# Kernel tuning notes

Measured on AMD Instinct MI355X. Metric: run time of the kernel, lower is better.

The kernel has to match this reference:

```python
import jax, jax.numpy as jnp
import numpy as np


def log_g(x):
    # log of g(x) = where(x>=0, x+0.5, sigmoid(x)) in log space
    return jnp.where(x >= 0, jnp.log(jax.nn.relu(x) + 0.5), -jax.nn.softplus(-x))


def setup_inputs() -> dict:
    key = jax.random.key(0)
    k1, k2, k3 = jax.random.split(key, 3)
    B, S, D = 4, 4096, 2048
    D_INNER = int(D * 1.5)  # 3072
    x = jax.random.normal(k1, (B, S, D), dtype=jnp.float32)
    w_hg = jax.random.normal(k2, (D, 2 * D_INNER), dtype=jnp.float32) * (D ** -0.5)
    w_out = jax.random.normal(k3, (D_INNER, D), dtype=jnp.float32) * (D_INNER ** -0.5)
    return {"x": x, "w_hg": w_hg, "w_out": w_out}


def reference(x, w_hg, w_out):
    # x: [B,S,D]; w_hg: [D, 2*Di]; w_out: [Di, D]
    hg = jnp.einsum('bsd,de->bse', x, w_hg)
    hidden, gate = jnp.split(hg, 2, axis=-1)  # each [B,S,Di]
    log_coeffs = -jax.nn.softplus(gate)        # log(1 - z)
    log_z = -jax.nn.softplus(-gate)            # log z
    log_values = log_z + log_g(hidden)
    # Heinsen associative scan in log space along seq axis
    a_star = jnp.cumsum(log_coeffs, axis=1)
    log_h = a_star + jax.lax.cumlogsumexp(log_values - a_star, axis=1)
    h = jnp.exp(log_h)                         # [B,S,Di]
    out = jnp.einsum('bse,ed->bsd', h, w_out)  # to_out Linear (expansion != 1)
    return out
```

## Files before the change

### kernel.cpp

```cpp
#include <hip/hip_runtime.h>
#include <hip/hip_bf16.h>
#include <stdint.h>

typedef __hip_bfloat16 bf16;
typedef __attribute__((ext_vector_type(8))) short short8;
typedef __attribute__((ext_vector_type(4))) float floatx4;
typedef __attribute__((address_space(3))) const unsigned short lu16;

__device__ __forceinline__ float ldf(const float* p) { return *p; }
__device__ __forceinline__ float ldf(const bf16* p) { return __bfloat162float(*p); }

__device__ __forceinline__ unsigned short f2bu(float f) {
  bf16 b = __float2bfloat16(f);
  return *reinterpret_cast<unsigned short*>(&b);
}

__device__ __forceinline__ void stnt(float* p, float v) { __builtin_nontemporal_store(v, p); }
__device__ __forceinline__ void stnt(bf16* p, float v) {
  __builtin_nontemporal_store(f2bu(v), (unsigned short*)p);
}

__device__ __forceinline__ void ld4(const float* p, float* o) {
  float4 v = *(const float4*)p;
  o[0] = v.x; o[1] = v.y; o[2] = v.z; o[3] = v.w;
}
__device__ __forceinline__ void ld4(const bf16* p, float* o) {
  ushort4 v = *(const ushort4*)p;
  o[0] = __bfloat162float(*(bf16*)&v.x);
  o[1] = __bfloat162float(*(bf16*)&v.y);
  o[2] = __bfloat162float(*(bf16*)&v.z);
  o[3] = __bfloat162float(*(bf16*)&v.w);
}

__device__ __forceinline__ void gl_lds16(const bf16* g, bf16* l) {
  __builtin_amdgcn_global_load_lds((const __attribute__((address_space(1))) void*)g,
                                   (__attribute__((address_space(3))) void*)l,
                                   16, 0, 0);
}

template <int OFF>
__device__ __forceinline__ short8 ldsro(lu16* p) {
  short8 r;
  asm volatile("ds_read_b128 %0, %1 offset:%2" : "=v"(r) : "v"(p), "i"(OFF));
  return r;
}

#define BAR() __builtin_amdgcn_s_barrier()
#define LGKM0() do { asm volatile("s_waitcnt lgkmcnt(0)" ::: "memory"); \
                     __builtin_amdgcn_sched_barrier(0); } while (0)
#define VMCNT(n) asm volatile("s_waitcnt vmcnt(" #n ")" ::: "memory")

__global__ void cvt_f32_bf16(const float* __restrict__ in, bf16* __restrict__ out, long n4) {
  long i = (long)blockIdx.x * blockDim.x + threadIdx.x;
  if (i >= n4) return;
  float4 v = ((const float4*)in)[i];
  ushort4 o;
  o.x = f2bu(v.x); o.y = f2bu(v.y); o.z = f2bu(v.z); o.w = f2bu(v.w);
  ((ushort4*)out)[i] = o;
}

__global__ void transpose_f32_to_bf16(const float* __restrict__ in, bf16* __restrict__ out,
                                      int R, int Cc) {
  __shared__ float tile[32][33];
  int tx = threadIdx.x & 31;
  int ty = threadIdx.x >> 5;
  int c0 = blockIdx.x * 32;
  int r0 = blockIdx.y * 32;
#pragma unroll
  for (int i = 0; i < 32; i += 8)
    tile[ty + i][tx] = in[(long)(r0 + ty + i) * Cc + c0 + tx];
  __syncthreads();
#pragma unroll
  for (int i = 0; i < 32; i += 8)
    out[(long)(c0 + ty + i) * R + r0 + tx] = __float2bfloat16(tile[tx][ty + i]);
}

template <typename OUT_T>
__global__ __launch_bounds__(512, 2) void gemm256(const bf16* __restrict__ A,
                                                  const bf16* __restrict__ BT,
                                                  OUT_T* __restrict__ C,
                                                  int M, int N, int K) {
  __shared__ __align__(16) bf16 lds[2][2][256][64];

  const int tid = threadIdx.x;
  const int w = tid >> 6;
  const int lane = tid & 63;
  const int quad = lane >> 4;
  const int r16 = lane & 15;
  const int wm = (w >> 2) * 128;
  const int wn = (w & 3) * 64;

  const int nbx = N >> 8;
  const int nwg = nbx * (M >> 8);
  const int bid = blockIdx.x;
  const int swz = (bid & 7) * (nwg >> 3) + (bid >> 3);
  const long bM = (long)(swz / nbx) * 256;
  const long bN = (long)(swz % nbx) * 256;

  const int r0 = tid >> 3;
  const int c8 = (tid & 7) ^ (r0 & 7);
  const bf16* Ag = A + (bM + r0) * (long)K + c8 * 8;
  const bf16* Bg = BT + (bN + r0) * (long)K + c8 * 8;
  const int lslot = w * 512;

  bf16* Am0 = &lds[0][0][0][0];
  bf16* Am1 = &lds[1][0][0][0];
  bf16* Bm0 = &lds[0][1][0][0];
  bf16* Bm1 = &lds[1][1][0][0];

  auto stage = [&](const bf16* g, bf16* lmat, int half, int kt) {
    const bf16* gs = g + (long)half * 128 * K + (long)kt * 64;
    bf16* ls = lmat + half * 8192 + lslot;
    gl_lds16(gs, ls);
    gl_lds16(gs + 64L * K, ls + 4096);
  };

  const int lofsA = (wm + r16) * 64;
  const int lofsB = (wn + r16) * 64;
  const int c8x0 = ((0 * 4 + quad) ^ (r16 & 7)) * 8;
  const int c8x1 = ((1 * 4 + quad) ^ (r16 & 7)) * 8;
  lu16* lb = (lu16*)&lds[0][0][0][0];
  lu16* pA0k0 = lb + 0 * 32768 + 0 * 16384 + lofsA + c8x0;
  lu16* pA0k1 = lb + 0 * 32768 + 0 * 16384 + lofsA + c8x1;
  lu16* pA1k0 = lb + 1 * 32768 + 0 * 16384 + lofsA + c8x0;
  lu16* pA1k1 = lb + 1 * 32768 + 0 * 16384 + lofsA + c8x1;
  lu16* pB0k0 = lb + 0 * 32768 + 1 * 16384 + lofsB + c8x0;
  lu16* pB0k1 = lb + 0 * 32768 + 1 * 16384 + lofsB + c8x1;
  lu16* pB1k0 = lb + 1 * 32768 + 1 * 16384 + lofsB + c8x0;
  lu16* pB1k1 = lb + 1 * 32768 + 1 * 16384 + lofsB + c8x1;

  floatx4 acc[8][4];
#pragma unroll
  for (int a = 0; a < 8; a++)
#pragma unroll
    for (int b = 0; b < 4; b++) acc[a][b] = (floatx4){0.f, 0.f, 0.f, 0.f};

  short8 af[4][2], bq0[2][2], bq1[2][2];

#define READ_A(P0, P1, MG) do { \
  af[0][0] = ldsro<((MG)*4 + 0) * 2048>(P0); af[0][1] = ldsro<((MG)*4 + 0) * 2048>(P1); \
  af[1][0] = ldsro<((MG)*4 + 1) * 2048>(P0); af[1][1] = ldsro<((MG)*4 + 1) * 2048>(P1); \
  af[2][0] = ldsro<((MG)*4 + 2) * 2048>(P0); af[2][1] = ldsro<((MG)*4 + 2) * 2048>(P1); \
  af[3][0] = ldsro<((MG)*4 + 3) * 2048>(P0); af[3][1] = ldsro<((MG)*4 + 3) * 2048>(P1); \
} while (0)

#define READ_B(P0, P1, NG, BQ) do { \
  BQ[0][0] = ldsro<((NG)*2 + 0) * 2048>(P0); BQ[0][1] = ldsro<((NG)*2 + 0) * 2048>(P1); \
  BQ[1][0] = ldsro<((NG)*2 + 1) * 2048>(P0); BQ[1][1] = ldsro<((NG)*2 + 1) * 2048>(P1); \
} while (0)

#define PH_MMA(MG, NG, BQ) do { \
  __builtin_amdgcn_s_setprio(1); \
  _Pragma("unroll") \
  for (int mf = 0; mf < 4; ++mf) \
    _Pragma("unroll") \
    for (int nf = 0; nf < 2; ++nf) { \
      acc[(MG)*4 + mf][(NG)*2 + nf] = __builtin_amdgcn_mfma_f32_16x16x32_bf16( \
          af[mf][0], BQ[nf][0], acc[(MG)*4 + mf][(NG)*2 + nf], 0, 0, 0); \
      acc[(MG)*4 + mf][(NG)*2 + nf] = __builtin_amdgcn_mfma_f32_16x16x32_bf16( \
          af[mf][1], BQ[nf][1], acc[(MG)*4 + mf][(NG)*2 + nf], 0, 0, 0); \
    } \
  __builtin_amdgcn_s_setprio(0); \
} while (0)

#define KTILE(PA0, PA1, PB0, PB1, S1, S2, S3, S4, VMX) do { \
  READ_A(PA0, PA1, 0); READ_B(PB0, PB1, 0, bq0); S1; \
  BAR(); LGKM0(); PH_MMA(0, 0, bq0); BAR(); \
  READ_B(PB0, PB1, 1, bq1); S2; \
  BAR(); LGKM0(); PH_MMA(0, 1, bq1); BAR(); \
  READ_A(PA0, PA1, 1); S3; \
  BAR(); LGKM0(); PH_MMA(1, 1, bq1); BAR(); \
  S4; BAR(); PH_MMA(1, 0, bq0); VMX; BAR(); \
} while (0)

  stage(Ag, Am0, 0, 0); stage(Ag, Am0, 1, 0);
  stage(Bg, Bm0, 0, 0); stage(Bg, Bm0, 1, 0);
  stage(Bg, Bm1, 0, 1); stage(Bg, Bm1, 1, 1);
  VMCNT(4);
  BAR();

  const int NI = K >> 7;
  for (int i = 0; i < NI - 1; ++i) {
    const int k1 = 2 * i + 1, k2 = 2 * i + 2, k3 = 2 * i + 3;
    KTILE(pA0k0, pA0k1, pB0k0, pB0k1,
          stage(Ag, Am1, 0, k1), stage(Ag, Am1, 1, k1),
          stage(Bg, Bm0, 0, k2), stage(Bg, Bm0, 1, k2), VMCNT(4));
    KTILE(pA1k0, pA1k1, pB1k0, pB1k1,
          stage(Ag, Am0, 0, k2), stage(Ag, Am0, 1, k2),
          stage(Bg, Bm1, 0, k3), stage(Bg, Bm1, 1, k3), VMCNT(4));
  }
  {
    const int kl = 2 * NI - 1;
    KTILE(pA0k0, pA0k1, pB0k0, pB0k1,
          stage(Ag, Am1, 0, kl), stage(Ag, Am1, 1, kl),
          (void)0, (void)0, VMCNT(0));
    KTILE(pA1k0, pA1k1, pB1k0, pB1k1,
          (void)0, (void)0, (void)0, (void)0, (void)0);
  }

#undef KTILE
#undef PH_MMA
#undef READ_B
#undef READ_A

#pragma unroll
  for (int mf = 0; mf < 8; ++mf) {
#pragma unroll
    for (int i2 = 0; i2 < 4; ++i2) {
      long row = bM + wm + mf * 16 + quad * 4 + i2;
      OUT_T* crow = C + row * (long)N + bN + wn + r16;
#pragma unroll
      for (int nf = 0; nf < 4; ++nf) stnt(&crow[nf * 16], acc[mf][nf][i2]);
    }
  }
}

__device__ __forceinline__ void cv_compute(float hval, float gval, float& c, float& v) {
  float eg = __expf(gval);
  c = 1.f / (1.f + eg);
  float z = 1.f - c;
  float gx = (hval >= 0.f) ? (hval + 0.5f) : (1.f / (1.f + __expf(-hval)));
  v = z * gx;
}

template <typename T>
__global__ void scan_pass1(const T* __restrict__ hg, float* __restrict__ P,
                           float* __restrict__ V, int S, int Di, int NN, int nch) {
  int tid = blockIdx.x * blockDim.x + threadIdx.x;
  int De = Di >> 2;
  int e = (tid % De) * 4;
  int rest = tid / De;
  int ch = rest % nch;
  int b = rest / nch;
  int CH = S / nch;
  const T* ph = hg + ((long)(b * S + ch * CH)) * NN + e;
  float Pv[4] = {1.f, 1.f, 1.f, 1.f}, Vv[4] = {0.f, 0.f, 0.f, 0.f};
  for (int t = 0; t < CH; t++) {
    float hv[4], gv[4];
    ld4(ph, hv);
    ld4(ph + Di, gv);
#pragma unroll
    for (int j = 0; j < 4; j++) {
      float c, v;
      cv_compute(hv[j], gv[j], c, v);
      Pv[j] *= c;
      Vv[j] = fmaf(c, Vv[j], v);
    }
    ph += NN;
  }
  long base = ((long)(b * nch + ch)) * Di + e;
  *(float4*)&P[base] = make_float4(Pv[0], Pv[1], Pv[2], Pv[3]);
  *(float4*)&V[base] = make_float4(Vv[0], Vv[1], Vv[2], Vv[3]);
}

__global__ void scan_pass2(const float* __restrict__ P, const float* __restrict__ V,
                           float* __restrict__ Hc, int Di, int nch) {
  int tid = blockIdx.x * blockDim.x + threadIdx.x;
  int e = tid % Di;
  int b = tid / Di;
  float H = 0.f;
  for (int j = 0; j < nch; j++) {
    long idx = ((long)(b * nch + j)) * Di + e;
    Hc[idx] = H;
    H = fmaf(P[idx], H, V[idx]);
  }
}

template <typename T>
__global__ void scan_pass3(const T* __restrict__ hg, const float* __restrict__ Hc,
                           bf16* __restrict__ h, int S, int Di, int NN, int nch) {
  int tid = blockIdx.x * blockDim.x + threadIdx.x;
  int De = Di >> 2;
  int e = (tid % De) * 4;
  int rest = tid / De;
  int ch = rest % nch;
  int b = rest / nch;
  int CH = S / nch;
  const T* ph = hg + ((long)(b * S + ch * CH)) * NN + e;
  bf16* po = h + ((long)(b * S + ch * CH)) * Di + e;
  long base = ((long)(b * nch + ch)) * Di + e;
  float4 hc = *(const float4*)&Hc[base];
  float H[4] = {hc.x, hc.y, hc.z, hc.w};
  for (int t = 0; t < CH; t++) {
    float hv[4], gv[4];
    ld4(ph, hv);
    ld4(ph + Di, gv);
    ushort4 o;
#pragma unroll
    for (int j = 0; j < 4; j++) {
      float c, v;
      cv_compute(hv[j], gv[j], c, v);
      H[j] = fmaf(c, H[j], v);
    }
    o.x = f2bu(H[0]); o.y = f2bu(H[1]); o.z = f2bu(H[2]); o.w = f2bu(H[3]);
    *(ushort4*)po = o;
    ph += NN;
    po += Di;
  }
}

extern "C" void kernel_launch(void* const* d_in, const int* in_sizes, int n_in,
                              void* d_out, int out_size, void* d_ws, size_t ws_size,
                              hipStream_t stream) {
  const int B = 4, S = 4096, D = 2048, Di = 3072, NN = 6144;
  const int Mr = B * S;
  const int NCH = 32;

  const float* x = (const float*)d_in[0];
  const float* w_hg = (const float*)d_in[1];
  const float* w_out = (const float*)d_in[2];
  float* out = (float*)d_out;

  char* wp = (char*)d_ws;
  bf16* x_bf = (bf16*)wp;  wp += (size_t)Mr * D * 2;
  bf16* whgT = (bf16*)wp;  wp += (size_t)NN * D * 2;
  bf16* woutT = (bf16*)wp; wp += (size_t)D * Di * 2;
  bf16* h_bf = (bf16*)wp;  wp += (size_t)Mr * Di * 2;
  float* P = (float*)wp;   wp += (size_t)B * NCH * Di * 4;
  float* V = (float*)wp;   wp += (size_t)B * NCH * Di * 4;
  float* Hc = (float*)wp;  wp += (size_t)B * NCH * Di * 4;
  size_t used = (size_t)(wp - (char*)d_ws);
  bool f32hg = (used + (size_t)Mr * NN * 4) <= ws_size;
  void* hgp = (void*)wp;

  cvt_f32_bf16<<<(int)(((long)Mr * D / 4 + 255) / 256), 256, 0, stream>>>(x, x_bf, (long)Mr * D / 4);
  transpose_f32_to_bf16<<<dim3(NN / 32, D / 32), 256, 0, stream>>>(w_hg, whgT, D, NN);
  transpose_f32_to_bf16<<<dim3(D / 32, Di / 32), 256, 0, stream>>>(w_out, woutT, Di, D);

  const int nwg1 = (NN / 256) * (Mr / 256);
  const int nwg2 = (D / 256) * (Mr / 256);
  int scan_vthreads = B * NCH * (Di / 4);

  if (f32hg) {
    float* hg = (float*)hgp;
    gemm256<float><<<nwg1, 512, 0, stream>>>(x_bf, whgT, hg, Mr, NN, D);
    scan_pass1<float><<<scan_vthreads / 256, 256, 0, stream>>>(hg, P, V, S, Di, NN, NCH);
    scan_pass2<<<(B * Di) / 256, 256, 0, stream>>>(P, V, Hc, Di, NCH);
    scan_pass3<float><<<scan_vthreads / 256, 256, 0, stream>>>(hg, Hc, h_bf, S, Di, NN, NCH);
  } else {
    bf16* hg = (bf16*)hgp;
    gemm256<bf16><<<nwg1, 512, 0, stream>>>(x_bf, whgT, hg, Mr, NN, D);
    scan_pass1<bf16><<<scan_vthreads / 256, 256, 0, stream>>>(hg, P, V, S, Di, NN, NCH);
    scan_pass2<<<(B * Di) / 256, 256, 0, stream>>>(P, V, Hc, Di, NCH);
    scan_pass3<bf16><<<scan_vthreads / 256, 256, 0, stream>>>(hg, Hc, h_bf, S, Di, NN, NCH);
  }

  gemm256<float><<<nwg2, 512, 0, stream>>>(h_bf, woutT, out, Mr, D, Di);
}
```

Measured before the change: 1.023 ms.

## Always store hg as bf16, rebalance GEMM staging, double scan chunks

Removes the fp32 hg path so the first GEMM always writes bf16 and the scan passes read half the bytes. It also reschedules the GEMM's global-to-LDS staging so one A sub-tile load is issued a phase earlier, with the wait count raised from 4 to 6. Epilogue stores change from nontemporal to regular stores, scan chunks go from 32 to 64, and the P/V/Hc buffers now reuse the x_bf workspace. The cost is lower precision in hg and a shift in the GEMM's prefetch depth and LDS timing.

Measured after the change: 951.7 us. 7.0% less time.

```diff
diff --git a/kernel.cpp b/kernel.cpp
--- a/kernel.cpp
+++ b/kernel.cpp
@@ -7,23 +7,14 @@
 typedef __attribute__((ext_vector_type(4))) float floatx4;
 typedef __attribute__((address_space(3))) const unsigned short lu16;
 
-__device__ __forceinline__ float ldf(const float* p) { return *p; }
-__device__ __forceinline__ float ldf(const bf16* p) { return __bfloat162float(*p); }
-
 __device__ __forceinline__ unsigned short f2bu(float f) {
   bf16 b = __float2bfloat16(f);
   return *reinterpret_cast<unsigned short*>(&b);
 }
 
-__device__ __forceinline__ void stnt(float* p, float v) { __builtin_nontemporal_store(v, p); }
-__device__ __forceinline__ void stnt(bf16* p, float v) {
-  __builtin_nontemporal_store(f2bu(v), (unsigned short*)p);
-}
-
-__device__ __forceinline__ void ld4(const float* p, float* o) {
-  float4 v = *(const float4*)p;
-  o[0] = v.x; o[1] = v.y; o[2] = v.z; o[3] = v.w;
-}
+__device__ __forceinline__ void stf(float* p, float v) { *p = v; }
+__device__ __forceinline__ void stf(bf16* p, float v) { *p = __float2bfloat16(v); }
+
 __device__ __forceinline__ void ld4(const bf16* p, float* o) {
   ushort4 v = *(const ushort4*)p;
   o[0] = __bfloat162float(*(bf16*)&v.x);
@@ -163,37 +154,40 @@
   __builtin_amdgcn_s_setprio(0); \
 } while (0)
 
-#define KTILE(PA0, PA1, PB0, PB1, S1, S2, S3, S4, VMX) do { \
+#define KTILE(PA0, PA1, PB0, PB1, S1, S3, S4a, S4b, VMX) do { \
   READ_A(PA0, PA1, 0); READ_B(PB0, PB1, 0, bq0); S1; \
   BAR(); LGKM0(); PH_MMA(0, 0, bq0); BAR(); \
-  READ_B(PB0, PB1, 1, bq1); S2; \
+  READ_B(PB0, PB1, 1, bq1); \
   BAR(); LGKM0(); PH_MMA(0, 1, bq1); BAR(); \
   READ_A(PA0, PA1, 1); S3; \
   BAR(); LGKM0(); PH_MMA(1, 1, bq1); BAR(); \
-  S4; BAR(); PH_MMA(1, 0, bq0); VMX; BAR(); \
+  S4a; S4b; BAR(); PH_MMA(1, 0, bq0); VMX; BAR(); \
 } while (0)
 
   stage(Ag, Am0, 0, 0); stage(Ag, Am0, 1, 0);
   stage(Bg, Bm0, 0, 0); stage(Bg, Bm0, 1, 0);
-  stage(Bg, Bm1, 0, 1); stage(Bg, Bm1, 1, 1);
-  VMCNT(4);
+  stage(Bg, Bm1, 0, 1);
+  stage(Bg, Bm1, 1, 1); stage(Ag, Am1, 0, 1);
+  VMCNT(6);
   BAR();
 
   const int NI = K >> 7;
   for (int i = 0; i < NI - 1; ++i) {
     const int k1 = 2 * i + 1, k2 = 2 * i + 2, k3 = 2 * i + 3;
     KTILE(pA0k0, pA0k1, pB0k0, pB0k1,
-          stage(Ag, Am1, 0, k1), stage(Ag, Am1, 1, k1),
-          stage(Bg, Bm0, 0, k2), stage(Bg, Bm0, 1, k2), VMCNT(4));
+          stage(Ag, Am1, 1, k1),
+          stage(Bg, Bm0, 0, k2),
+          stage(Bg, Bm0, 1, k2), stage(Ag, Am0, 0, k2), VMCNT(6));
     KTILE(pA1k0, pA1k1, pB1k0, pB1k1,
-          stage(Ag, Am0, 0, k2), stage(Ag, Am0, 1, k2),
-          stage(Bg, Bm1, 0, k3), stage(Bg, Bm1, 1, k3), VMCNT(4));
+          stage(Ag, Am0, 1, k2),
+          stage(Bg, Bm1, 0, k3),
+          stage(Bg, Bm1, 1, k3), stage(Ag, Am1, 0, k3), VMCNT(6));
   }
   {
     const int kl = 2 * NI - 1;
     KTILE(pA0k0, pA0k1, pB0k0, pB0k1,
-          stage(Ag, Am1, 0, kl), stage(Ag, Am1, 1, kl),
-          (void)0, (void)0, VMCNT(0));
+          stage(Ag, Am1, 1, kl),
+          (void)0, (void)0, (void)0, VMCNT(0));
     KTILE(pA1k0, pA1k1, pB1k0, pB1k1,
           (void)0, (void)0, (void)0, (void)0, (void)0);
   }
@@ -210,7 +204,7 @@
       long row = bM + wm + mf * 16 + quad * 4 + i2;
       OUT_T* crow = C + row * (long)N + bN + wn + r16;
 #pragma unroll
-      for (int nf = 0; nf < 4; ++nf) stnt(&crow[nf * 16], acc[mf][nf][i2]);
+      for (int nf = 0; nf < 4; ++nf) stf(&crow[nf * 16], acc[mf][nf][i2]);
     }
   }
 }
@@ -223,8 +217,7 @@
   v = z * gx;
 }
 
-template <typename T>
-__global__ void scan_pass1(const T* __restrict__ hg, float* __restrict__ P,
+__global__ void scan_pass1(const bf16* __restrict__ hg, float* __restrict__ P,
                            float* __restrict__ V, int S, int Di, int NN, int nch) {
   int tid = blockIdx.x * blockDim.x + threadIdx.x;
   int De = Di >> 2;
@@ -233,7 +226,7 @@
   int ch = rest % nch;
   int b = rest / nch;
   int CH = S / nch;
-  const T* ph = hg + ((long)(b * S + ch * CH)) * NN + e;
+  const bf16* ph = hg + ((long)(b * S + ch * CH)) * NN + e;
   float Pv[4] = {1.f, 1.f, 1.f, 1.f}, Vv[4] = {0.f, 0.f, 0.f, 0.f};
   for (int t = 0; t < CH; t++) {
     float hv[4], gv[4];
@@ -266,8 +259,7 @@
   }
 }
 
-template <typename T>
-__global__ void scan_pass3(const T* __restrict__ hg, const float* __restrict__ Hc,
+__global__ void scan_pass3(const bf16* __restrict__ hg, const float* __restrict__ Hc,
                            bf16* __restrict__ h, int S, int Di, int NN, int nch) {
   int tid = blockIdx.x * blockDim.x + threadIdx.x;
   int De = Di >> 2;
@@ -276,7 +268,7 @@
   int ch = rest % nch;
   int b = rest / nch;
   int CH = S / nch;
-  const T* ph = hg + ((long)(b * S + ch * CH)) * NN + e;
+  const bf16* ph = hg + ((long)(b * S + ch * CH)) * NN + e;
   bf16* po = h + ((long)(b * S + ch * CH)) * Di + e;
   long base = ((long)(b * nch + ch)) * Di + e;
   float4 hc = *(const float4*)&Hc[base];
@@ -304,7 +296,7 @@
                               hipStream_t stream) {
   const int B = 4, S = 4096, D = 2048, Di = 3072, NN = 6144;
   const int Mr = B * S;
-  const int NCH = 32;
+  const int NCH = 64;
 
   const float* x = (const float*)d_in[0];
   const float* w_hg = (const float*)d_in[1];
@@ -316,12 +308,11 @@
   bf16* whgT = (bf16*)wp;  wp += (size_t)NN * D * 2;
   bf16* woutT = (bf16*)wp; wp += (size_t)D * Di * 2;
   bf16* h_bf = (bf16*)wp;  wp += (size_t)Mr * Di * 2;
-  float* P = (float*)wp;   wp += (size_t)B * NCH * Di * 4;
-  float* V = (float*)wp;   wp += (size_t)B * NCH * Di * 4;
-  float* Hc = (float*)wp;  wp += (size_t)B * NCH * Di * 4;
-  size_t used = (size_t)(wp - (char*)d_ws);
-  bool f32hg = (used + (size_t)Mr * NN * 4) <= ws_size;
-  void* hgp = (void*)wp;
+  bf16* hg = (bf16*)wp;    wp += (size_t)Mr * NN * 2;
+
+  float* P = (float*)x_bf;
+  float* V = P + (size_t)B * NCH * Di;
+  float* Hc = V + (size_t)B * NCH * Di;
 
   cvt_f32_bf16<<<(int)(((long)Mr * D / 4 + 255) / 256), 256, 0, stream>>>(x, x_bf, (long)Mr * D / 4);
   transpose_f32_to_bf16<<<dim3(NN / 32, D / 32), 256, 0, stream>>>(w_hg, whgT, D, NN);
@@ -331,19 +322,10 @@
   const int nwg2 = (D / 256) * (Mr / 256);
   int scan_vthreads = B * NCH * (Di / 4);
 
-  if (f32hg) {
-    float* hg = (float*)hgp;
-    gemm256<float><<<nwg1, 512, 0, stream>>>(x_bf, whgT, hg, Mr, NN, D);
-    scan_pass1<float><<<scan_vthreads / 256, 256, 0, stream>>>(hg, P, V, S, Di, NN, NCH);
-    scan_pass2<<<(B * Di) / 256, 256, 0, stream>>>(P, V, Hc, Di, NCH);
-    scan_pass3<float><<<scan_vthreads / 256, 256, 0, stream>>>(hg, Hc, h_bf, S, Di, NN, NCH);
-  } else {
-    bf16* hg = (bf16*)hgp;
-    gemm256<bf16><<<nwg1, 512, 0, stream>>>(x_bf, whgT, hg, Mr, NN, D);
-    scan_pass1<bf16><<<scan_vthreads / 256, 256, 0, stream>>>(hg, P, V, S, Di, NN, NCH);
-    scan_pass2<<<(B * Di) / 256, 256, 0, stream>>>(P, V, Hc, Di, NCH);
-    scan_pass3<bf16><<<scan_vthreads / 256, 256, 0, stream>>>(hg, Hc, h_bf, S, Di, NN, NCH);
-  }
+  gemm256<bf16><<<nwg1, 512, 0, stream>>>(x_bf, whgT, hg, Mr, NN, D);
+  scan_pass1<<<scan_vthreads / 256, 256, 0, stream>>>(hg, P, V, S, Di, NN, NCH);
+  scan_pass2<<<(B * Di) / 256, 256, 0, stream>>>(P, V, Hc, Di, NCH);
+  scan_pass3<<<scan_vthreads / 256, 256, 0, stream>>>(hg, Hc, h_bf, S, Di, NN, NCH);
 
   gemm256<float><<<nwg2, 512, 0, stream>>>(h_bf, woutT, out, Mr, D, Di);
 }
```
